# Performance work log

Measured on AMD Instinct MI355X. Metric: run time of the kernel, lower is better.

The kernel has to match this reference:

```python
import jax, jax.numpy as jnp
import numpy as np


def setup_inputs() -> dict:
    key = jax.random.key(0)
    kq, kk, kv = jax.random.split(key, 3)
    B, H, N, D = 4, 16, 2048, 64
    q = jax.random.normal(kq, (B, H, N, D), dtype=jnp.float32)
    k = jax.random.normal(kk, (B, N, D), dtype=jnp.float32)
    v = jax.random.normal(kv, (B, N, D), dtype=jnp.float32)
    return {"q": q, "k": k, "v": v}


def reference(q, k, v):
    # q: [B,H,N,D], k/v: [B,N,D] (KV shared across heads)
    scale = q.shape[-1] ** -0.5
    sim = jnp.einsum('bhid,bjd->bhij', q, k) * scale  # [B,H,N,N]
    attn = jax.nn.softmax(sim, axis=-1)
    return jnp.einsum('bhij,bjd->bhid', attn, v)  # [B,H,N,D]
```

## Files before the change

### kernel.cpp

```cpp
#include <hip/hip_runtime.h>
#include <hip/hip_bf16.h>

#define B_ 4
#define H_ 16
#define N_ 2048
#define D_ 64
#define BM 256
#define BN 64

typedef __bf16 bf16;
typedef bf16 bf16x4 __attribute__((ext_vector_type(4)));
typedef bf16 bf16x8 __attribute__((ext_vector_type(8)));
typedef float f32x2 __attribute__((ext_vector_type(2)));
typedef float f32x16 __attribute__((ext_vector_type(16)));
typedef unsigned u32x2 __attribute__((ext_vector_type(2)));
typedef unsigned u32x4 __attribute__((ext_vector_type(4)));

#define SCALE_LOG2E 0.18033688011112042f

#define GBL(p) ((const __attribute__((address_space(1))) void*)(p))
#define LDS(p) ((__attribute__((address_space(3))) void*)(p))

__global__ __launch_bounds__(256) void convert_kv(const float* __restrict__ k,
                                                  const float* __restrict__ v,
                                                  bf16* __restrict__ img) {
    const int tile = blockIdx.x >> 1;
    const int b = tile >> 5, T = tile & 31;
    const int pu = (blockIdx.x & 1) * 256 + threadIdx.x;
    const int mtks = pu >> 6;
    const int ln   = pu & 63;
    const int mt = mtks >> 2, ks = mtks & 3;
    bf16* timg = img + (size_t)tile * 8192;

    {
        const int kvr = T * 64 + mt * 32 + (ln & 31);
        const int d0  = ks * 16 + (ln >> 5) * 8;
        const float* src = k + ((size_t)b * N_ + kvr) * D_ + d0;
        float4 a = *(const float4*)src;
        float4 c = *(const float4*)(src + 4);
        bf16x8 o;
        o[0] = (bf16)a.x; o[1] = (bf16)a.y; o[2] = (bf16)a.z; o[3] = (bf16)a.w;
        o[4] = (bf16)c.x; o[5] = (bf16)c.y; o[6] = (bf16)c.z; o[7] = (bf16)c.w;
        *(bf16x8*)(timg + pu * 8) = o;
    }
    {
        const int d   = mt * 32 + (ln & 31);
        const int kv0 = T * 64 + ks * 16 + (ln >> 5) * 8;
        const float* src = v + ((size_t)b * N_ + kv0) * D_ + d;
        bf16x8 o;
        #pragma unroll
        for (int j = 0; j < 8; ++j) o[j] = (bf16)src[(size_t)j * D_];
        *(bf16x8*)(timg + 4096 + pu * 8) = o;
    }
}

static __device__ inline bf16x4 pack4(float a, float b, float c, float d) {
    bf16x4 r; r[0] = (bf16)a; r[1] = (bf16)b; r[2] = (bf16)c; r[3] = (bf16)d; return r;
}

static __device__ inline bf16x8 cswap(bf16x4 lo, bf16x4 hi) {
    u32x2 l = __builtin_bit_cast(u32x2, lo);
    u32x2 h = __builtin_bit_cast(u32x2, hi);
    u32x2 r0 = __builtin_amdgcn_permlane32_swap(l[0], h[0], false, false);
    u32x2 r1 = __builtin_amdgcn_permlane32_swap(l[1], h[1], false, false);
    u32x4 o; o[0] = r0[0]; o[1] = r1[0]; o[2] = r0[1]; o[3] = r1[1];
    return __builtin_bit_cast(bf16x8, o);
}

__global__ __launch_bounds__(512, 2) void attn_fwd(const float* __restrict__ q,
                                                   const bf16* __restrict__ img,
                                                   float* __restrict__ out) {
    __shared__ __align__(16) bf16 KV[2][2][8192];
    __shared__ float EXL[8][64];

    const int tid  = threadIdx.x;
    const int lane = tid & 63;
    const int wv   = tid >> 6;
    const int grp  = wv >> 2;
    const int wp   = wv & 3;
    const int half = lane >> 5;
    const int l31  = lane & 31;

    const int bh = blockIdx.y;
    const int b  = bh >> 4;
    const int q0 = blockIdx.x * BM + wp * 64;

    const bf16* tiles = img + (size_t)b * 32 * 8192;

    bf16x8 qf[2][4];
    #pragma unroll
    for (int qn = 0; qn < 2; ++qn)
        #pragma unroll
        for (int ks = 0; ks < 4; ++ks) {
            const float* src = q + ((size_t)bh * N_ + q0 + qn * 32 + l31) * D_ + ks * 16 + half * 8;
            float4 a = *(const float4*)src;
            float4 c = *(const float4*)(src + 4);
            bf16x8 pk;
            pk[0] = (bf16)(a.x * SCALE_LOG2E); pk[1] = (bf16)(a.y * SCALE_LOG2E);
            pk[2] = (bf16)(a.z * SCALE_LOG2E); pk[3] = (bf16)(a.w * SCALE_LOG2E);
            pk[4] = (bf16)(c.x * SCALE_LOG2E); pk[5] = (bf16)(c.y * SCALE_LOG2E);
            pk[6] = (bf16)(c.z * SCALE_LOG2E); pk[7] = (bf16)(c.w * SCALE_LOG2E);
            qf[qn][ks] = pk;
        }

    f32x16 acc[2][2] = {{{}, {}}, {{}, {}}};
    float lacc[2] = {0.f, 0.f};

    auto issue_dma = [&](int t, int p) {
        const bf16* g = tiles + (size_t)t * 8192;
        #pragma unroll
        for (int j = 0; j < 4; ++j) {
            const int c = wp * 4 + j;
            __builtin_amdgcn_global_load_lds(GBL(g + c * 512 + lane * 8),
                                             LDS(&KV[grp][p][c * 512]), 16, 0, 0);
        }
    };

    const int t0 = grp * 16;
    issue_dma(t0, 0);

    for (int it = 0; it < 16; ++it) {
        const int p = it & 1;
        __syncthreads();
        if (it + 1 < 16) issue_dma(t0 + it + 1, p ^ 1);

        bf16x8 kf[2][4], vf[2][4];
        #pragma unroll
        for (int mt = 0; mt < 2; ++mt)
            #pragma unroll
            for (int ks = 0; ks < 4; ++ks) {
                kf[mt][ks] = *(const bf16x8*)&KV[grp][p][((mt * 4 + ks) * 64 + lane) * 8];
                vf[mt][ks] = *(const bf16x8*)&KV[grp][p][4096 + ((mt * 4 + ks) * 64 + lane) * 8];
            }

        #pragma unroll
        for (int qn = 0; qn < 2; ++qn) {
            f32x16 s[2] = {{}, {}};
            #pragma unroll
            for (int ks = 0; ks < 4; ++ks) {
                s[0] = __builtin_amdgcn_mfma_f32_32x32x16_bf16(kf[0][ks], qf[qn][ks], s[0], 0, 0, 0);
                s[1] = __builtin_amdgcn_mfma_f32_32x32x16_bf16(kf[1][ks], qf[qn][ks], s[1], 0, 0, 0);
            }
            #pragma unroll
            for (int mt = 0; mt < 2; ++mt) {
                float pv[16];
                #pragma unroll
                for (int r = 0; r < 16; ++r) pv[r] = __builtin_amdgcn_exp2f(s[mt][r]);
                float t0s = 0.f, t1s = 0.f;
                #pragma unroll
                for (int r = 0; r < 8; ++r) { t0s += pv[r]; t1s += pv[8 + r]; }
                lacc[qn] += t0s + t1s;
                #pragma unroll
                for (int sp = 0; sp < 2; ++sp) {
                    bf16x4 lo = pack4(pv[8 * sp + 0], pv[8 * sp + 1], pv[8 * sp + 2], pv[8 * sp + 3]);
                    bf16x4 hi = pack4(pv[8 * sp + 4], pv[8 * sp + 5], pv[8 * sp + 6], pv[8 * sp + 7]);
                    bf16x8 bfrag = cswap(lo, hi);
                    const int g = mt * 2 + sp;
                    acc[0][qn] = __builtin_amdgcn_mfma_f32_32x32x16_bf16(vf[0][g], bfrag, acc[0][qn], 0, 0, 0);
                    acc[1][qn] = __builtin_amdgcn_mfma_f32_32x32x16_bf16(vf[1][g], bfrag, acc[1][qn], 0, 0, 0);
                }
            }
        }
    }

    __syncthreads();
    float* ex = (float*)&KV[0][0][0] + wp * 4096;

    if (grp == 1) {
        #pragma unroll
        for (int mt = 0; mt < 2; ++mt)
            #pragma unroll
            for (int qn = 0; qn < 2; ++qn)
                #pragma unroll
                for (int rq = 0; rq < 4; ++rq) {
                    const int c = (mt * 2 + qn) * 4 + rq;
                    float4 v4;
                    v4.x = acc[mt][qn][4 * rq + 0];
                    v4.y = acc[mt][qn][4 * rq + 1];
                    v4.z = acc[mt][qn][4 * rq + 2];
                    v4.w = acc[mt][qn][4 * rq + 3];
                    *(float4*)&ex[(c * 64 + lane) * 4] = v4;
                }
        EXL[wp * 2 + 0][lane] = lacc[0];
        EXL[wp * 2 + 1][lane] = lacc[1];
    }
    __syncthreads();
    if (grp == 0) {
        lacc[0] += EXL[wp * 2 + 0][lane];
        lacc[1] += EXL[wp * 2 + 1][lane];
        #pragma unroll
        for (int mt = 0; mt < 2; ++mt)
            #pragma unroll
            for (int qn = 0; qn < 2; ++qn)
                #pragma unroll
                for (int rq = 0; rq < 4; ++rq) {
                    const int c = (mt * 2 + qn) * 4 + rq;
                    float4 v4 = *(const float4*)&ex[(c * 64 + lane) * 4];
                    acc[mt][qn][4 * rq + 0] += v4.x;
                    acc[mt][qn][4 * rq + 1] += v4.y;
                    acc[mt][qn][4 * rq + 2] += v4.z;
                    acc[mt][qn][4 * rq + 3] += v4.w;
                }

        #pragma unroll
        for (int qn = 0; qn < 2; ++qn) {
            float l = lacc[qn] + __shfl_xor(lacc[qn], 32);
            float inv = 1.0f / l;
            const int qrow = q0 + qn * 32 + l31;
            float* dst = out + ((size_t)bh * N_ + qrow) * D_ + 4 * half;
            #pragma unroll
            for (int mt = 0; mt < 2; ++mt)
                #pragma unroll
                for (int rq = 0; rq < 4; ++rq) {
                    float4 o;
                    o.x = acc[mt][qn][4 * rq + 0] * inv;
                    o.y = acc[mt][qn][4 * rq + 1] * inv;
                    o.z = acc[mt][qn][4 * rq + 2] * inv;
                    o.w = acc[mt][qn][4 * rq + 3] * inv;
                    *(float4*)(dst + mt * 32 + 8 * rq) = o;
                }
        }
    }
}

extern "C" void kernel_launch(void* const* d_in, const int* in_sizes, int n_in,
                              void* d_out, int out_size, void* d_ws, size_t ws_size,
                              hipStream_t stream) {
    const float* q = (const float*)d_in[0];
    const float* k = (const float*)d_in[1];
    const float* v = (const float*)d_in[2];
    float* out = (float*)d_out;

    bf16* img = (bf16*)d_ws;

    convert_kv<<<B_ * 64, 256, 0, stream>>>(k, v, img);
    dim3 grid(N_ / BM, B_ * H_);
    attn_fwd<<<grid, 512, 0, stream>>>(q, img, out);
}
```

Before: 156.1 us.

## Halve query tile per wave and raise occupancy to four blocks per CU

Each wave now processes 32 query rows instead of 64, so BM drops to 128 and the grid doubles. K/V fragments are loaded from LDS right before each MFMA instead of being held in registers, which cuts register pressure enough to allow launch_bounds(512,4). The convert kernel is split so K and V conversion run in separate blocks. The cost is that each K/V tile loaded into LDS is reused across half as many queries, so global-to-LDS traffic and LDS reads per unit of compute roughly double.

Result: slower. 159.4 us (+2.1%).

```diff
diff --git a/kernel.cpp b/kernel.cpp
--- a/kernel.cpp
+++ b/kernel.cpp
@@ -5,7 +5,7 @@
 #define H_ 16
 #define N_ 2048
 #define D_ 64
-#define BM 256
+#define BM 128
 #define BN 64
 
 typedef __bf16 bf16;
@@ -24,15 +24,16 @@
 __global__ __launch_bounds__(256) void convert_kv(const float* __restrict__ k,
                                                   const float* __restrict__ v,
                                                   bf16* __restrict__ img) {
-    const int tile = blockIdx.x >> 1;
+    const int tile = blockIdx.x >> 2;
+    const int part = blockIdx.x & 3;
     const int b = tile >> 5, T = tile & 31;
-    const int pu = (blockIdx.x & 1) * 256 + threadIdx.x;
+    const int pu = (part & 1) * 256 + threadIdx.x;
     const int mtks = pu >> 6;
     const int ln   = pu & 63;
     const int mt = mtks >> 2, ks = mtks & 3;
     bf16* timg = img + (size_t)tile * 8192;
 
-    {
+    if (part < 2) {
         const int kvr = T * 64 + mt * 32 + (ln & 31);
         const int d0  = ks * 16 + (ln >> 5) * 8;
         const float* src = k + ((size_t)b * N_ + kvr) * D_ + d0;
@@ -42,8 +43,7 @@
         o[0] = (bf16)a.x; o[1] = (bf16)a.y; o[2] = (bf16)a.z; o[3] = (bf16)a.w;
         o[4] = (bf16)c.x; o[5] = (bf16)c.y; o[6] = (bf16)c.z; o[7] = (bf16)c.w;
         *(bf16x8*)(timg + pu * 8) = o;
-    }
-    {
+    } else {
         const int d   = mt * 32 + (ln & 31);
         const int kv0 = T * 64 + ks * 16 + (ln >> 5) * 8;
         const float* src = v + ((size_t)b * N_ + kv0) * D_ + d;
@@ -67,11 +67,11 @@
     return __builtin_bit_cast(bf16x8, o);
 }
 
-__global__ __launch_bounds__(512, 2) void attn_fwd(const float* __restrict__ q,
+__global__ __launch_bounds__(512, 4) void attn_fwd(const float* __restrict__ q,
                                                    const bf16* __restrict__ img,
                                                    float* __restrict__ out) {
     __shared__ __align__(16) bf16 KV[2][2][8192];
-    __shared__ float EXL[8][64];
+    __shared__ float EXL[4][64];
 
     const int tid  = threadIdx.x;
     const int lane = tid & 63;
@@ -83,28 +83,26 @@
 
     const int bh = blockIdx.y;
     const int b  = bh >> 4;
-    const int q0 = blockIdx.x * BM + wp * 64;
+    const int q0 = blockIdx.x * BM + wp * 32;
 
     const bf16* tiles = img + (size_t)b * 32 * 8192;
 
-    bf16x8 qf[2][4];
+    bf16x8 qf[4];
     #pragma unroll
-    for (int qn = 0; qn < 2; ++qn)
-        #pragma unroll
-        for (int ks = 0; ks < 4; ++ks) {
-            const float* src = q + ((size_t)bh * N_ + q0 + qn * 32 + l31) * D_ + ks * 16 + half * 8;
-            float4 a = *(const float4*)src;
-            float4 c = *(const float4*)(src + 4);
-            bf16x8 pk;
-            pk[0] = (bf16)(a.x * SCALE_LOG2E); pk[1] = (bf16)(a.y * SCALE_LOG2E);
-            pk[2] = (bf16)(a.z * SCALE_LOG2E); pk[3] = (bf16)(a.w * SCALE_LOG2E);
-            pk[4] = (bf16)(c.x * SCALE_LOG2E); pk[5] = (bf16)(c.y * SCALE_LOG2E);
-            pk[6] = (bf16)(c.z * SCALE_LOG2E); pk[7] = (bf16)(c.w * SCALE_LOG2E);
-            qf[qn][ks] = pk;
-        }
-
-    f32x16 acc[2][2] = {{{}, {}}, {{}, {}}};
-    float lacc[2] = {0.f, 0.f};
+    for (int ks = 0; ks < 4; ++ks) {
+        const float* src = q + ((size_t)bh * N_ + q0 + l31) * D_ + ks * 16 + half * 8;
+        float4 a = *(const float4*)src;
+        float4 c = *(const float4*)(src + 4);
+        bf16x8 pk;
+        pk[0] = (bf16)(a.x * SCALE_LOG2E); pk[1] = (bf16)(a.y * SCALE_LOG2E);
+        pk[2] = (bf16)(a.z * SCALE_LOG2E); pk[3] = (bf16)(a.w * SCALE_LOG2E);
+        pk[4] = (bf16)(c.x * SCALE_LOG2E); pk[5] = (bf16)(c.y * SCALE_LOG2E);
+        pk[6] = (bf16)(c.z * SCALE_LOG2E); pk[7] = (bf16)(c.w * SCALE_LOG2E);
+        qf[ks] = pk;
+    }
+
+    f32x16 acc[2] = {{}, {}};
+    float lacc = 0.f;
 
     auto issue_dma = [&](int t, int p) {
         const bf16* g = tiles + (size_t)t * 8192;
@@ -124,102 +122,85 @@
         __syncthreads();
         if (it + 1 < 16) issue_dma(t0 + it + 1, p ^ 1);
 
-        bf16x8 kf[2][4], vf[2][4];
+        f32x16 s[2] = {{}, {}};
+        #pragma unroll
+        for (int ks = 0; ks < 4; ++ks) {
+            bf16x8 k0 = *(const bf16x8*)&KV[grp][p][((0 * 4 + ks) * 64 + lane) * 8];
+            bf16x8 k1 = *(const bf16x8*)&KV[grp][p][((1 * 4 + ks) * 64 + lane) * 8];
+            s[0] = __builtin_amdgcn_mfma_f32_32x32x16_bf16(k0, qf[ks], s[0], 0, 0, 0);
+            s[1] = __builtin_amdgcn_mfma_f32_32x32x16_bf16(k1, qf[ks], s[1], 0, 0, 0);
+        }
+        #pragma unroll
+        for (int mt = 0; mt < 2; ++mt) {
+            float pv[16];
+            #pragma unroll
+            for (int r = 0; r < 16; ++r) pv[r] = __builtin_amdgcn_exp2f(s[mt][r]);
+            float t0s = 0.f, t1s = 0.f;
+            #pragma unroll
+            for (int r = 0; r < 8; ++r) { t0s += pv[r]; t1s += pv[8 + r]; }
+            lacc += t0s + t1s;
+            #pragma unroll
+            for (int sp = 0; sp < 2; ++sp) {
+                bf16x4 lo = pack4(pv[8 * sp + 0], pv[8 * sp + 1], pv[8 * sp + 2], pv[8 * sp + 3]);
+                bf16x4 hi = pack4(pv[8 * sp + 4], pv[8 * sp + 5], pv[8 * sp + 6], pv[8 * sp + 7]);
+                bf16x8 bfrag = cswap(lo, hi);
+                const int g = mt * 2 + sp;
+                bf16x8 v0 = *(const bf16x8*)&KV[grp][p][4096 + ((0 * 4 + g) * 64 + lane) * 8];
+                bf16x8 v1 = *(const bf16x8*)&KV[grp][p][4096 + ((1 * 4 + g) * 64 + lane) * 8];
+                acc[0] = __builtin_amdgcn_mfma_f32_32x32x16_bf16(v0, bfrag, acc[0], 0, 0, 0);
+                acc[1] = __builtin_amdgcn_mfma_f32_32x32x16_bf16(v1, bfrag, acc[1], 0, 0, 0);
+            }
+        }
+    }
+
+    __syncthreads();
+    float* ex = (float*)&KV[0][0][0] + wp * 2048;
+
+    if (grp == 1) {
         #pragma unroll
         for (int mt = 0; mt < 2; ++mt)
             #pragma unroll
-            for (int ks = 0; ks < 4; ++ks) {
-                kf[mt][ks] = *(const bf16x8*)&KV[grp][p][((mt * 4 + ks) * 64 + lane) * 8];
-                vf[mt][ks] = *(const bf16x8*)&KV[grp][p][4096 + ((mt * 4 + ks) * 64 + lane) * 8];
-            }
-
-        #pragma unroll
-        for (int qn = 0; qn < 2; ++qn) {
-            f32x16 s[2] = {{}, {}};
-            #pragma unroll
-            for (int ks = 0; ks < 4; ++ks) {
-                s[0] = __builtin_amdgcn_mfma_f32_32x32x16_bf16(kf[0][ks], qf[qn][ks], s[0], 0, 0, 0);
-                s[1] = __builtin_amdgcn_mfma_f32_32x32x16_bf16(kf[1][ks], qf[qn][ks], s[1], 0, 0, 0);
-            }
-            #pragma unroll
-            for (int mt = 0; mt < 2; ++mt) {
-                float pv[16];
-                #pragma unroll
-                for (int r = 0; r < 16; ++r) pv[r] = __builtin_amdgcn_exp2f(s[mt][r]);
-                float t0s = 0.f, t1s = 0.f;
-                #pragma unroll
-                for (int r = 0; r < 8; ++r) { t0s += pv[r]; t1s += pv[8 + r]; }
-                lacc[qn] += t0s + t1s;
-                #pragma unroll
-                for (int sp = 0; sp < 2; ++sp) {
-                    bf16x4 lo = pack4(pv[8 * sp + 0], pv[8 * sp + 1], pv[8 * sp + 2], pv[8 * sp + 3]);
-                    bf16x4 hi = pack4(pv[8 * sp + 4], pv[8 * sp + 5], pv[8 * sp + 6], pv[8 * sp + 7]);
-                    bf16x8 bfrag = cswap(lo, hi);
-                    const int g = mt * 2 + sp;
-                    acc[0][qn] = __builtin_amdgcn_mfma_f32_32x32x16_bf16(vf[0][g], bfrag, acc[0][qn], 0, 0, 0);
-                    acc[1][qn] = __builtin_amdgcn_mfma_f32_32x32x16_bf16(vf[1][g], bfrag, acc[1][qn], 0, 0, 0);
-                }
-            }
-        }
-    }
-
-    __syncthreads();
-    float* ex = (float*)&KV[0][0][0] + wp * 4096;
-
-    if (grp == 1) {
-        #pragma unroll
-        for (int mt = 0; mt < 2; ++mt)
-            #pragma unroll
-            for (int qn = 0; qn < 2; ++qn)
-                #pragma unroll
-                for (int rq = 0; rq < 4; ++rq) {
-                    const int c = (mt * 2 + qn) * 4 + rq;
-                    float4 v4;
-                    v4.x = acc[mt][qn][4 * rq + 0];
-                    v4.y = acc[mt][qn][4 * rq + 1];
-                    v4.z = acc[mt][qn][4 * rq + 2];
-                    v4.w = acc[mt][qn][4 * rq + 3];
-                    *(float4*)&ex[(c * 64 + lane) * 4] = v4;
-                }
-        EXL[wp * 2 + 0][lane] = lacc[0];
-        EXL[wp * 2 + 1][lane] = lacc[1];
+            for (int rq = 0; rq < 4; ++rq) {
+                const int c = mt * 4 + rq;
+                float4 v4;
+                v4.x = acc[mt][4 * rq + 0];
+                v4.y = acc[mt][4 * rq + 1];
+                v4.z = acc[mt][4 * rq + 2];
+                v4.w = acc[mt][4 * rq + 3];
+                *(float4*)&ex[(c * 64 + lane) * 4] = v4;
+            }
+        EXL[wp][lane] = lacc;
     }
     __syncthreads();
     if (grp == 0) {
-        lacc[0] += EXL[wp * 2 + 0][lane];
-        lacc[1] += EXL[wp * 2 + 1][lane];
+        lacc += EXL[wp][lane];
         #pragma unroll
         for (int mt = 0; mt < 2; ++mt)
             #pragma unroll
-            for (int qn = 0; qn < 2; ++qn)
-                #pragma unroll
-                for (int rq = 0; rq < 4; ++rq) {
-                    const int c = (mt * 2 + qn) * 4 + rq;
-                    float4 v4 = *(const float4*)&ex[(c * 64 + lane) * 4];
-                    acc[mt][qn][4 * rq + 0] += v4.x;
-                    acc[mt][qn][4 * rq + 1] += v4.y;
-                    acc[mt][qn][4 * rq + 2] += v4.z;
-                    acc[mt][qn][4 * rq + 3] += v4.w;
-                }
-
-        #pragma unroll
-        for (int qn = 0; qn < 2; ++qn) {
-            float l = lacc[qn] + __shfl_xor(lacc[qn], 32);
-            float inv = 1.0f / l;
-            const int qrow = q0 + qn * 32 + l31;
-            float* dst = out + ((size_t)bh * N_ + qrow) * D_ + 4 * half;
-            #pragma unroll
-            for (int mt = 0; mt < 2; ++mt)
-                #pragma unroll
-                for (int rq = 0; rq < 4; ++rq) {
-                    float4 o;
-                    o.x = acc[mt][qn][4 * rq + 0] * inv;
-                    o.y = acc[mt][qn][4 * rq + 1] * inv;
-                    o.z = acc[mt][qn][4 * rq + 2] * inv;
-                    o.w = acc[mt][qn][4 * rq + 3] * inv;
-                    *(float4*)(dst + mt * 32 + 8 * rq) = o;
-                }
-        }
+            for (int rq = 0; rq < 4; ++rq) {
+                const int c = mt * 4 + rq;
+                float4 v4 = *(const float4*)&ex[(c * 64 + lane) * 4];
+                acc[mt][4 * rq + 0] += v4.x;
+                acc[mt][4 * rq + 1] += v4.y;
+                acc[mt][4 * rq + 2] += v4.z;
+                acc[mt][4 * rq + 3] += v4.w;
+            }
+
+        float l = lacc + __shfl_xor(lacc, 32);
+        float inv = 1.0f / l;
+        const int qrow = q0 + l31;
+        float* dst = out + ((size_t)bh * N_ + qrow) * D_ + 4 * half;
+        #pragma unroll
+        for (int mt = 0; mt < 2; ++mt)
+            #pragma unroll
+            for (int rq = 0; rq < 4; ++rq) {
+                float4 o;
+                o.x = acc[mt][4 * rq + 0] * inv;
+                o.y = acc[mt][4 * rq + 1] * inv;
+                o.z = acc[mt][4 * rq + 2] * inv;
+                o.w = acc[mt][4 * rq + 3] * inv;
+                *(float4*)(dst + mt * 32 + 8 * rq) = o;
+            }
     }
 }
 
@@ -233,7 +214,7 @@
 
     bf16* img = (bf16*)d_ws;
 
-    convert_kv<<<B_ * 64, 256, 0, stream>>>(k, v, img);
+    convert_kv<<<B_ * 128, 256, 0, stream>>>(k, v, img);
     dim3 grid(N_ / BM, B_ * H_);
     attn_fwd<<<grid, 512, 0, stream>>>(q, img, out);
 }
```
